# Optimization experiments

Measured on AMD Instinct MI355X. Metric: run time of the kernel, lower is better.

## Reference

```python
import jax, jax.numpy as jnp
import numpy as np
import math

D_MODEL, D_INNER, D_STATE, D_CONV, DT_RANK = 768, 1536, 16, 4, 48
BATCH, SEQLEN = 2, 1024
DT_MIN, DT_MAX = 1e-4, 1.0


def setup_inputs() -> dict:
    key = jax.random.key(0)
    ks = jax.random.split(key, 10)
    D, N, R, K = D_INNER, D_STATE, DT_RANK, D_CONV
    total_out = 2 * D + R + 2 * D * N

    def xavier(k, shape):
        fan_in, fan_out = shape[1], shape[0]
        a = math.sqrt(6.0 / (fan_in + fan_out))
        return jax.random.uniform(k, shape, jnp.float32, -a, a)

    x = jax.random.normal(ks[0], (BATCH, SEQLEN, D_MODEL), jnp.float32)
    W_in = xavier(ks[1], (total_out, D_MODEL))
    W_dt = xavier(ks[2], (D, R))
    W_out = xavier(ks[3], (D_MODEL, D))
    W_res = xavier(ks[4], (D, D_MODEL))
    conv_w = jax.random.normal(ks[5], (D, K), jnp.float32) * (1.0 / math.sqrt(K))
    conv_b = jnp.zeros((D,), jnp.float32)
    # A_log init: log(1..N) per inner channel
    A_log = jnp.broadcast_to(jnp.log(jnp.arange(1, N + 1, dtype=jnp.float32)), (D, N))
    Dskip = jnp.ones((D,), jnp.float32)
    # dt_bias = inverse_softplus(exp(uniform in [log dt_min, log dt_max]))
    dt = jnp.exp(jax.random.uniform(ks[6], (D,), jnp.float32) * (math.log(DT_MAX) - math.log(DT_MIN)) + math.log(DT_MIN))
    dt_bias = dt + jnp.log(-jnp.expm1(-dt))
    norm_w = jnp.ones((D,), jnp.float32)
    ln_w = jnp.ones((D_MODEL,), jnp.float32)
    ln_b = jnp.zeros((D_MODEL,), jnp.float32)
    return {
        "x": x, "ln_w": ln_w, "ln_b": ln_b, "W_in": W_in, "W_dt": W_dt,
        "conv_w": conv_w, "conv_b": conv_b, "A_log": A_log, "Dskip": Dskip,
        "dt_bias": dt_bias, "norm_w": norm_w, "W_res": W_res, "W_out": W_out,
    }


def _forward(x, ln_w, ln_b, W_in, W_dt, conv_w, conv_b, A_log, Dskip, dt_bias, norm_w, W_res, W_out):
    B, L, _ = x.shape
    D, N = A_log.shape
    K = conv_w.shape[1]
    R = W_dt.shape[1]
    # pre LayerNorm
    mu = x.mean(-1, keepdims=True)
    var = ((x - mu) ** 2).mean(-1, keepdims=True)
    xn = (x - mu) * jax.lax.rsqrt(var + 1e-5) * ln_w + ln_b
    # fused input projection, then split
    p = jnp.einsum('bld,od->blo', xn, W_in)  # (B,L,2D+R+2DN)
    z = p[..., :D]
    u = p[..., D:2 * D]
    dth = p[..., 2 * D:2 * D + R]
    Bpar = p[..., 2 * D + R:2 * D + R + D * N].reshape(B, L, D, N)
    Cpar = p[..., 2 * D + R + D * N:].reshape(B, L, D, N)
    # causal depthwise conv over time on u
    uc = jax.lax.conv_general_dilated(
        u.transpose(0, 2, 1), conv_w[:, None, :], (1,), [(K - 1, 0)],
        feature_group_count=D, dimension_numbers=('NCH', 'OIH', 'NCH'))
    u = (uc + conv_b[None, :, None]).transpose(0, 2, 1)  # (B,L,D)
    # dt: low-rank proj + bias -> softplus -> clamp
    dt = jnp.clip(jax.nn.softplus(jnp.einsum('blr,dr->bld', dth, W_dt) + dt_bias), DT_MIN, DT_MAX)
    A = -jnp.exp(A_log)  # (D,N), negative
    dA = jnp.exp(dt[..., None] * A)          # (B,L,D,N)
    dBu = (dt * u)[..., None] * Bpar         # (B,L,D,N)

    def step(h, inp):
        dA_t, dBu_t, C_t = inp               # each (B,D,N)
        h = dA_t * h + dBu_t
        return h, (C_t * h).sum(-1)          # y_t: (B,D)

    h0 = jnp.zeros((B, D, N), x.dtype)
    _, ys = jax.lax.scan(step, h0, (dA.transpose(1, 0, 2, 3),
                                    dBu.transpose(1, 0, 2, 3),
                                    Cpar.transpose(1, 0, 2, 3)))
    y = ys.transpose(1, 0, 2) + u * Dskip    # (B,L,D)
    # fused gated RMSNorm + inner residual
    res = jnp.einsum('blm,dm->bld', x, W_res)
    g = y * jax.nn.silu(z)
    g = g * jax.lax.rsqrt((g * g).mean(-1, keepdims=True) + 1e-6) * norm_w + res
    return jnp.einsum('bld,md->blm', g, W_out)


def reference(x, ln_w, ln_b, W_in, W_dt, conv_w, conv_b, A_log, Dskip, dt_bias, norm_w, W_res, W_out):
    return _forward(x, ln_w, ln_b, W_in, W_dt, conv_w, conv_b, A_log, Dskip, dt_bias, norm_w, W_res, W_out)
```

## Files before the change

### kernel.cpp

```cpp
#include <hip/hip_runtime.h>


typedef unsigned short u16;
typedef __bf16 bf16x8 __attribute__((ext_vector_type(8)));
typedef float f32x4 __attribute__((ext_vector_type(4)));

#define OPAD 52480
#define OTOT 52272
#define DI   1536
#define DM   768
#define Z0   0
#define U0   1536
#define DTH0 3072
#define B0   3120
#define C0   27696

#define SCAN_P 64
#define SCAN_T 16
#define SPF    4

__device__ static inline u16 f2bf(float f) {
    unsigned u = __float_as_uint(f);
    u += 0x7fffu + ((u >> 16) & 1u);
    return (u16)(u >> 16);
}
__device__ static inline float bf2f(u16 s) {
    return __uint_as_float(((unsigned)s) << 16);
}

__device__ static inline void gload16(const void* g, void* l) {
    __builtin_amdgcn_global_load_lds(
        (const __attribute__((address_space(1))) unsigned int*)g,
        (__attribute__((address_space(3))) unsigned int*)l, 16, 0, 0);
}

__device__ static inline void unpack8(uint4 v, float* f) {
    unsigned w0 = v.x, w1 = v.y, w2 = v.z, w3 = v.w;
    f[0] = __uint_as_float(w0 << 16); f[1] = __uint_as_float(w0 & 0xffff0000u);
    f[2] = __uint_as_float(w1 << 16); f[3] = __uint_as_float(w1 & 0xffff0000u);
    f[4] = __uint_as_float(w2 << 16); f[5] = __uint_as_float(w2 & 0xffff0000u);
    f[6] = __uint_as_float(w3 << 16); f[7] = __uint_as_float(w3 & 0xffff0000u);
}

__global__ void cvt_kernel(const float* __restrict__ src, u16* __restrict__ dst,
                           long n_src, long n_tot) {
    long i4 = ((long)blockIdx.x * 256 + threadIdx.x) * 4;
    if (i4 >= n_tot) return;
    ushort4 o;
    if (i4 < n_src) {
        float4 v = *(const float4*)(src + i4);
        o.x = f2bf(v.x); o.y = f2bf(v.y); o.z = f2bf(v.z); o.w = f2bf(v.w);
    } else {
        o.x = o.y = o.z = o.w = 0;
    }
    *(ushort4*)(dst + i4) = o;
}

__device__ static inline void block_reduce2(float& a, float& b) {
    #pragma unroll
    for (int o = 32; o > 0; o >>= 1) {
        a += __shfl_down(a, o);
        b += __shfl_down(b, o);
    }
    __shared__ float sa[4], sb[4];
    int lane = threadIdx.x & 63, w = threadIdx.x >> 6;
    if (lane == 0) { sa[w] = a; sb[w] = b; }
    __syncthreads();
    a = sa[0] + sa[1] + sa[2] + sa[3];
    b = sb[0] + sb[1] + sb[2] + sb[3];
}

__global__ void __launch_bounds__(256) ln_kernel(const float* __restrict__ x,
        const float* __restrict__ w, const float* __restrict__ b,
        u16* __restrict__ xnbf, u16* __restrict__ xbf) {
    int m = blockIdx.x, tid = threadIdx.x;
    const float* xr = x + (size_t)m * DM;
    float v[3];
    v[0] = xr[tid]; v[1] = xr[tid + 256]; v[2] = xr[tid + 512];
    float s = v[0] + v[1] + v[2];
    float ss = v[0]*v[0] + v[1]*v[1] + v[2]*v[2];
    block_reduce2(s, ss);
    float mu = s * (1.f / DM);
    float var = ss * (1.f / DM) - mu * mu;
    float inv = rsqrtf(var + 1e-5f);
    #pragma unroll
    for (int i = 0; i < 3; ++i) {
        int d = tid + i * 256;
        float xn = (v[i] - mu) * inv * w[d] + b[d];
        xnbf[(size_t)m * DM + d] = f2bf(xn);
        xbf[(size_t)m * DM + d] = f2bf(v[i]);
    }
}

template <int OUT_BF16>
__global__ void __launch_bounds__(256) gemm_bt(const u16* __restrict__ A,
        const u16* __restrict__ B, void* __restrict__ C, int K, int ldc) {
    __shared__ u16 smem[2 * 128 * 64];
    u16* As = smem;
    u16* Bs = smem + 128 * 64;
    int tid = threadIdx.x;
    int m0 = blockIdx.x * 128, n0 = blockIdx.y * 128;
    int lane = tid & 63, wave = tid >> 6;
    int wm = wave >> 1, wn = wave & 1;
    int l15 = lane & 15, l4 = lane >> 4;
    f32x4 acc[4][4] = {};
    const u16* Ag = A + (size_t)m0 * K;
    const u16* Bg = B + (size_t)n0 * K;
    int crow = tid >> 3;
    int ccol = ((tid & 7) ^ ((tid >> 3) & 7)) * 8;
    int ldsoff = (tid & 192) * 16;
    int xr = l15 & 7;

    for (int k0 = 0; k0 < K; k0 += 64) {
        __syncthreads();
        #pragma unroll
        for (int it = 0; it < 4; ++it) {
            gload16(Ag + (size_t)(it * 32 + crow) * K + k0 + ccol,
                    (char*)As + it * 4096 + ldsoff);
            gload16(Bg + (size_t)(it * 32 + crow) * K + k0 + ccol,
                    (char*)Bs + it * 4096 + ldsoff);
        }
        __syncthreads();
        const u16* Arow = As + (wm * 64 + l15) * 64;
        const u16* Brow = Bs + (wn * 64 + l15) * 64;
        #pragma unroll
        for (int kk8 = 0; kk8 < 8; kk8 += 4) {
            int sw = ((l4 + kk8) ^ xr) * 8;
            bf16x8 af[4], bfr[4];
            #pragma unroll
            for (int i = 0; i < 4; ++i) af[i] = *(const bf16x8*)(Arow + i * 16 * 64 + sw);
            #pragma unroll
            for (int j = 0; j < 4; ++j) bfr[j] = *(const bf16x8*)(Brow + j * 16 * 64 + sw);
            #pragma unroll
            for (int i = 0; i < 4; ++i)
                #pragma unroll
                for (int j = 0; j < 4; ++j)
                    acc[i][j] = __builtin_amdgcn_mfma_f32_16x16x32_bf16(
                        af[i], bfr[j], acc[i][j], 0, 0, 0);
        }
    }
    #pragma unroll
    for (int i = 0; i < 4; ++i) {
        int row = m0 + wm * 64 + i * 16 + l4 * 4;
        #pragma unroll
        for (int j = 0; j < 4; ++j) {
            int col = n0 + wn * 64 + j * 16 + l15;
            #pragma unroll
            for (int r = 0; r < 4; ++r) {
                size_t off = (size_t)(row + r) * ldc + col;
                if (OUT_BF16) ((u16*)C)[off] = f2bf(acc[i][j][r]);
                else          ((float*)C)[off] = acc[i][j][r];
            }
        }
    }
}

#define G2_BUF  65536
#define G2_HALF 16384
#define G2_BOFF 32768

__global__ void __launch_bounds__(512, 2) gemm256_bt(const u16* __restrict__ A,
        const u16* __restrict__ B, u16* __restrict__ C, int K, int ldc) {
    __shared__ u16 smem[65536];
    char* smemc = (char*)smem;
    const int tid = threadIdx.x;
    const int l = tid & 63, w = tid >> 6;
    const int wm = w >> 2, wn = w & 3;
    const int l15 = l & 15, l4 = l >> 4;
    const int flat = blockIdx.y * 8 + blockIdx.x;
    const int wg = (flat & 7) * 205 + (flat >> 3);
    const int m0 = (wg & 7) * 256, n0 = (wg >> 3) * 256;
    const int NT = K >> 6;

    const int rA = l15 >> 1;
    const int rdoff = rA * 128 + ((((l4 << 1) + (l15 & 1)) ^ ((rA & 3) << 1)) << 4);
    const int wpr = (l & 7) ^ (((l >> 3) & 3) << 1);
    const int srow = w * 32 + ((l >> 3) << 1) + (wpr & 1);
    const u16* Ast = A + (size_t)(m0 + srow) * K + (wpr >> 1) * 8;
    const u16* Bst = B + (size_t)(n0 + srow) * K + (wpr >> 1) * 8;
    const int sdst = w * 2048;

    f32x4 acc[8][4] = {};
    bf16x8 bvK[4];

#define G2_STAGE(MATP, MOFF, nxt, sh, tk)                                      \
    gload16(MATP + (size_t)(tk) * 64 + (sh) * 32,                              \
            smemc + (nxt) * G2_BUF + (MOFF) + (sh) * G2_HALF + sdst);          \
    gload16(MATP + (size_t)16 * K + (size_t)(tk) * 64 + (sh) * 32,             \
            smemc + (nxt) * G2_BUF + (MOFF) + (sh) * G2_HALF + sdst + 1024);

#define G2_PHASE(cur, nxt, rh, h, READB, SMAT, SMOFF, sh, tk, DO_VM)           \
    {                                                                          \
        G2_STAGE(SMAT, SMOFF, nxt, sh, tk);                                    \
        const char* Ab = smemc + (cur) * G2_BUF + (h) * G2_HALF                \
                         + (wm * 128 + (rh) * 64) * 64 + rdoff;                \
        bf16x8 af[4];                                                          \
        if (READB) {                                                           \
            const char* Bb = smemc + (cur) * G2_BUF + G2_BOFF + (h) * G2_HALF  \
                             + (wn * 64) * 64 + rdoff;                         \
            _Pragma("unroll")                                                  \
            for (int j = 0; j < 4; ++j)                                        \
                bvK[j] = *(const bf16x8*)(Bb + j * 1024);                      \
        }                                                                      \
        _Pragma("unroll")                                                      \
        for (int i = 0; i < 4; ++i) af[i] = *(const bf16x8*)(Ab + i * 1024);   \
        __builtin_amdgcn_s_barrier();                                          \
        __builtin_amdgcn_s_setprio(1);                                         \
        _Pragma("unroll")                                                      \
        for (int i = 0; i < 4; ++i)                                            \
            _Pragma("unroll")                                                  \
            for (int j = 0; j < 4; ++j)                                        \
                acc[(rh) * 4 + i][j] = __builtin_amdgcn_mfma_f32_16x16x32_bf16(\
                    af[i], bvK[j], acc[(rh) * 4 + i][j], 0, 0, 0);             \
        __builtin_amdgcn_s_setprio(0);                                         \
        if (DO_VM) asm volatile("s_waitcnt vmcnt(4)" ::: "memory");            \
        __builtin_amdgcn_s_barrier();                                          \
    }

#define G2_TILE(cur, nxt, tk)                                                  \
    G2_PHASE(cur, nxt, 0, 0, 1, Ast, 0,       0, tk, 0)                        \
    G2_PHASE(cur, nxt, 1, 0, 0, Bst, G2_BOFF, 0, tk, 1)                        \
    G2_PHASE(cur, nxt, 0, 1, 1, Ast, 0,       1, tk, 0)                        \
    G2_PHASE(cur, nxt, 1, 1, 0, Bst, G2_BOFF, 1, tk, 1)

    G2_STAGE(Ast, 0,       0, 0, 0);
    G2_STAGE(Bst, G2_BOFF, 0, 0, 0);
    G2_STAGE(Ast, 0,       0, 1, 0);
    G2_STAGE(Bst, G2_BOFF, 0, 1, 0);
    asm volatile("s_waitcnt vmcnt(4)" ::: "memory");
    __builtin_amdgcn_s_barrier();

    for (int t = 0; t < NT; t += 2) {
        int tk1 = t + 1;
        int tk2 = (t + 2 < NT) ? t + 2 : NT - 1;
        G2_TILE(0, 1, tk1)
        G2_TILE(1, 0, tk2)
    }

    #pragma unroll
    for (int ai = 0; ai < 8; ++ai) {
        int row = m0 + wm * 128 + ai * 16 + l4 * 4;
        #pragma unroll
        for (int j = 0; j < 4; ++j) {
            int col = n0 + wn * 64 + j * 16 + l15;
            #pragma unroll
            for (int r = 0; r < 4; ++r)
                C[(size_t)(row + r) * ldc + col] = f2bf(acc[ai][j][r]);
        }
    }
#undef G2_STAGE
#undef G2_PHASE
#undef G2_TILE
}

__global__ void __launch_bounds__(256) dt_kernel(const u16* __restrict__ p,
        const float* __restrict__ Wdt, const float* __restrict__ dt_bias,
        float* __restrict__ dt) {
    int m0 = blockIdx.x * 16, tid = threadIdx.x;
    __shared__ float dth_s[16 * 48];
    for (int i = tid; i < 16 * 48; i += 256)
        dth_s[i] = bf2f(p[(size_t)(m0 + i / 48) * OPAD + DTH0 + (i % 48)]);
    __syncthreads();
    #pragma unroll
    for (int ii = 0; ii < 6; ++ii) {
        int d = ii * 256 + tid;
        float base = dt_bias[d];
        float acc[16];
        #pragma unroll
        for (int mm = 0; mm < 16; ++mm) acc[mm] = base;
        for (int r = 0; r < 48; ++r) {
            float wv = Wdt[d * 48 + r];
            #pragma unroll
            for (int mm = 0; mm < 16; ++mm)
                acc[mm] = fmaf(wv, dth_s[mm * 48 + r], acc[mm]);
        }
        #pragma unroll
        for (int mm = 0; mm < 16; ++mm) {
            float xv = acc[mm];
            float sp = xv > 20.f ? xv : log1pf(__expf(xv));
            sp = fminf(fmaxf(sp, 1e-4f), 1.0f);
            dt[(size_t)(m0 + mm) * DI + d] = sp;
        }
    }
}

__global__ void __launch_bounds__(256, 2) scan1_kernel(const u16* __restrict__ p,
        const float* __restrict__ dt, const float* __restrict__ A_log,
        const float* __restrict__ cw, const float* __restrict__ cb,
        float* __restrict__ chkA, float* __restrict__ chkB) {
    int d = blockIdx.x * 256 + threadIdx.x;
    int b = blockIdx.y, c = blockIdx.z;
    int t0base = c * SCAN_T;
    float a[16];
    #pragma unroll
    for (int n = 0; n < 16; ++n) a[n] = -__expf(A_log[d * 16 + n]);
    float cw0 = cw[d*4], cw1 = cw[d*4+1], cw2 = cw[d*4+2], cw3 = cw[d*4+3];
    float cbv = cb[d];
    const u16* pB = p + (size_t)(b * 1024 + t0base) * OPAD + B0 + d * 16;
    const u16* pU = p + (size_t)(b * 1024 + t0base) * OPAD + U0 + d;
    const float* dtp = dt + (size_t)(b * 1024 + t0base) * DI + d;
    float x1, x2, x3;
    if (c == 0) { x1 = x2 = x3 = 0.f; }
    else {
        x1 = bf2f(*(pU - (long)OPAD));
        x2 = bf2f(*(pU - 2L * OPAD));
        x3 = bf2f(*(pU - 3L * OPAD));
    }
    uint4 Br[SPF][2]; float dtr[SPF], xur[SPF];
    #pragma unroll
    for (int i = 0; i < SPF; ++i) {
        Br[i][0] = *(const uint4*)(pB + (size_t)i * OPAD);
        Br[i][1] = *(const uint4*)(pB + (size_t)i * OPAD + 8);
        dtr[i] = dtp[(size_t)i * DI];
        xur[i] = bf2f(pU[(size_t)i * OPAD]);
    }
    float h[16], Av[16];
    #pragma unroll
    for (int n = 0; n < 16; ++n) { h[n] = 0.f; Av[n] = 1.f; }
    for (int t0 = 0; t0 < SCAN_T; t0 += SPF) {
        #pragma unroll
        for (int s = 0; s < SPF; ++s) {
            int t = t0 + s;
            uint4 b0 = Br[s][0], b1 = Br[s][1];
            float dtv = dtr[s], xt = xur[s];
            int tl = t + SPF < SCAN_T ? t + SPF : SCAN_T - 1;
            Br[s][0] = *(const uint4*)(pB + (size_t)tl * OPAD);
            Br[s][1] = *(const uint4*)(pB + (size_t)tl * OPAD + 8);
            dtr[s] = dtp[(size_t)tl * DI];
            xur[s] = bf2f(pU[(size_t)tl * OPAD]);
            float uv = cbv;
            uv = fmaf(cw0, x3, uv);
            uv = fmaf(cw1, x2, uv);
            uv = fmaf(cw2, x1, uv);
            uv = fmaf(cw3, xt, uv);
            x3 = x2; x2 = x1; x1 = xt;
            float Bf[16];
            unpack8(b0, Bf); unpack8(b1, Bf + 8);
            float dtu = dtv * uv;
            #pragma unroll
            for (int n = 0; n < 16; ++n) {
                float dA = __expf(dtv * a[n]);
                h[n] = fmaf(dA, h[n], dtu * Bf[n]);
                Av[n] *= dA;
            }
        }
    }
    size_t o = (((size_t)c * 2 + b) * 1536 + d) * 16;
    #pragma unroll
    for (int k = 0; k < 4; ++k) {
        *(float4*)(chkA + o + k * 4) = make_float4(Av[4*k], Av[4*k+1], Av[4*k+2], Av[4*k+3]);
        *(float4*)(chkB + o + k * 4) = make_float4(h[4*k], h[4*k+1], h[4*k+2], h[4*k+3]);
    }
}

__global__ void __launch_bounds__(256) scan_comb_kernel(const float* __restrict__ chkA,
        const float* __restrict__ chkB, float* __restrict__ hstart) {
    int idx = blockIdx.x * 256 + threadIdx.x;
    float hs = 0.f;
    for (int c = 0; c < SCAN_P; ++c) {
        size_t o = (size_t)c * 49152 + idx;
        hstart[o] = hs;
        hs = fmaf(chkA[o], hs, chkB[o]);
    }
}

__global__ void __launch_bounds__(256, 2) scan2_kernel(const u16* __restrict__ p,
        const float* __restrict__ dt, const float* __restrict__ A_log,
        const float* __restrict__ cw, const float* __restrict__ cb,
        const float* __restrict__ Dskip,
        const float* __restrict__ hstart, float* __restrict__ y) {
    int d = blockIdx.x * 256 + threadIdx.x;
    int b = blockIdx.y, c = blockIdx.z;
    int t0base = c * SCAN_T;
    float a[16];
    #pragma unroll
    for (int n = 0; n < 16; ++n) a[n] = -__expf(A_log[d * 16 + n]);
    float Dsk = Dskip[d];
    float cw0 = cw[d*4], cw1 = cw[d*4+1], cw2 = cw[d*4+2], cw3 = cw[d*4+3];
    float cbv = cb[d];
    const u16* pB = p + (size_t)(b * 1024 + t0base) * OPAD + B0 + d * 16;
    const u16* pC = p + (size_t)(b * 1024 + t0base) * OPAD + C0 + d * 16;
    const u16* pU = p + (size_t)(b * 1024 + t0base) * OPAD + U0 + d;
    const float* dtp = dt + (size_t)(b * 1024 + t0base) * DI + d;
    float* yp        = y  + (size_t)(b * 1024 + t0base) * DI + d;
    float x1, x2, x3;
    if (c == 0) { x1 = x2 = x3 = 0.f; }
    else {
        x1 = bf2f(*(pU - (long)OPAD));
        x2 = bf2f(*(pU - 2L * OPAD));
        x3 = bf2f(*(pU - 3L * OPAD));
    }
    uint4 Br[SPF][2], Cr[SPF][2]; float dtr[SPF], xur[SPF];
    #pragma unroll
    for (int i = 0; i < SPF; ++i) {
        Br[i][0] = *(const uint4*)(pB + (size_t)i * OPAD);
        Br[i][1] = *(const uint4*)(pB + (size_t)i * OPAD + 8);
        Cr[i][0] = *(const uint4*)(pC + (size_t)i * OPAD);
        Cr[i][1] = *(const uint4*)(pC + (size_t)i * OPAD + 8);
        dtr[i] = dtp[(size_t)i * DI];
        xur[i] = bf2f(pU[(size_t)i * OPAD]);
    }
    float h[16];
    {
        size_t o = ((size_t)c * 3072 + (size_t)b * 1536 + d) * 16;
        #pragma unroll
        for (int k = 0; k < 4; ++k) {
            float4 hv = *(const float4*)(hstart + o + k * 4);
            h[4*k] = hv.x; h[4*k+1] = hv.y; h[4*k+2] = hv.z; h[4*k+3] = hv.w;
        }
    }
    for (int t0 = 0; t0 < SCAN_T; t0 += SPF) {
        #pragma unroll
        for (int s = 0; s < SPF; ++s) {
            int t = t0 + s;
            uint4 b0 = Br[s][0], b1 = Br[s][1], c0 = Cr[s][0], c1 = Cr[s][1];
            float dtv = dtr[s], xt = xur[s];
            int tl = t + SPF < SCAN_T ? t + SPF : SCAN_T - 1;
            Br[s][0] = *(const uint4*)(pB + (size_t)tl * OPAD);
            Br[s][1] = *(const uint4*)(pB + (size_t)tl * OPAD + 8);
            Cr[s][0] = *(const uint4*)(pC + (size_t)tl * OPAD);
            Cr[s][1] = *(const uint4*)(pC + (size_t)tl * OPAD + 8);
            dtr[s] = dtp[(size_t)tl * DI];
            xur[s] = bf2f(pU[(size_t)tl * OPAD]);
            float uv = cbv;
            uv = fmaf(cw0, x3, uv);
            uv = fmaf(cw1, x2, uv);
            uv = fmaf(cw2, x1, uv);
            uv = fmaf(cw3, xt, uv);
            x3 = x2; x2 = x1; x1 = xt;
            float Bf[16], Cf[16];
            unpack8(b0, Bf); unpack8(b1, Bf + 8);
            unpack8(c0, Cf); unpack8(c1, Cf + 8);
            float dtu = dtv * uv;
            #pragma unroll
            for (int n = 0; n < 16; ++n) {
                float dA = __expf(dtv * a[n]);
                h[n] = fmaf(dA, h[n], dtu * Bf[n]);
            }
            float a0 = fmaf(Cf[0], h[0], uv * Dsk), a1 = Cf[1] * h[1];
            float a2 = Cf[2] * h[2], a3 = Cf[3] * h[3];
            #pragma unroll
            for (int n = 4; n < 16; n += 4) {
                a0 = fmaf(Cf[n],   h[n],   a0);
                a1 = fmaf(Cf[n+1], h[n+1], a1);
                a2 = fmaf(Cf[n+2], h[n+2], a2);
                a3 = fmaf(Cf[n+3], h[n+3], a3);
            }
            yp[(size_t)t * DI] = (a0 + a1) + (a2 + a3);
        }
    }
}

__global__ void __launch_bounds__(256) gate_kernel(const u16* __restrict__ p,
        const float* __restrict__ y, const float* __restrict__ res,
        const float* __restrict__ norm_w, u16* __restrict__ g) {
    int m = blockIdx.x, tid = threadIdx.x;
    const u16* pz = p + (size_t)m * OPAD + Z0;
    const float* yr = y + (size_t)m * DI;
    float gp[6];
    float ss = 0.f, dummy = 0.f;
    #pragma unroll
    for (int i = 0; i < 6; ++i) {
        int d = i * 256 + tid;
        float z = bf2f(pz[d]);
        float gv = yr[d] * z / (1.f + __expf(-z));
        gp[i] = gv;
        ss += gv * gv;
    }
    block_reduce2(ss, dummy);
    float scale = rsqrtf(ss * (1.f / DI) + 1e-6f);
    #pragma unroll
    for (int i = 0; i < 6; ++i) {
        int d = i * 256 + tid;
        float val = gp[i] * scale * norm_w[d] + res[(size_t)m * DI + d];
        g[(size_t)m * DI + d] = f2bf(val);
    }
}

extern "C" void kernel_launch(void* const* d_in, const int* in_sizes, int n_in,
                              void* d_out, int out_size, void* d_ws, size_t ws_size,
                              hipStream_t stream) {
    const float* x       = (const float*)d_in[0];
    const float* ln_w    = (const float*)d_in[1];
    const float* ln_b    = (const float*)d_in[2];
    const float* W_in    = (const float*)d_in[3];
    const float* W_dt    = (const float*)d_in[4];
    const float* conv_w  = (const float*)d_in[5];
    const float* conv_b  = (const float*)d_in[6];
    const float* A_log   = (const float*)d_in[7];
    const float* Dskip   = (const float*)d_in[8];
    const float* dt_bias = (const float*)d_in[9];
    const float* norm_w  = (const float*)d_in[10];
    const float* W_res   = (const float*)d_in[11];
    const float* W_out   = (const float*)d_in[12];
    float* out = (float*)d_out;

    char* wsb = (char*)d_ws;
    u16* Wbf     = (u16*)(wsb + 0);
    u16* Wresbf  = (u16*)(wsb + 80609280);
    u16* Woutbf  = (u16*)(wsb + 82968576);
    u16* xnbf    = (u16*)(wsb + 85327872);
    u16* xbf     = (u16*)(wsb + 88473600);
    u16* pbuf    = (u16*)(wsb + 91619328);
    float* dtv   = (float*)(wsb + 319160320);
    float* ybuf  = (float*)(wsb + 331743232);
    float* resb  = (float*)(wsb + 344326144);
    u16* gbuf    = (u16*)(wsb + 356909056);
    float* chkA  = (float*)(wsb + 0);
    float* chkB  = (float*)(wsb + 12582912);
    float* hst   = (float*)(wsb + 25165824);

    cvt_kernel<<<39360, 256, 0, stream>>>(W_in, Wbf, (long)OTOT * DM, (long)OPAD * DM);
    cvt_kernel<<<1152, 256, 0, stream>>>(W_res, Wresbf, (long)DI * DM, (long)DI * DM);
    cvt_kernel<<<1152, 256, 0, stream>>>(W_out, Woutbf, (long)DM * DI, (long)DM * DI);
    ln_kernel<<<2048, 256, 0, stream>>>(x, ln_w, ln_b, xnbf, xbf);
    gemm256_bt<<<dim3(8, 205), 512, 0, stream>>>(xnbf, Wbf, pbuf, DM, OPAD);
    gemm_bt<0><<<dim3(16, 12), 256, 0, stream>>>(xbf, Wresbf, resb, DM, DI);
    dt_kernel<<<128, 256, 0, stream>>>(pbuf, W_dt, dt_bias, dtv);
    scan1_kernel<<<dim3(6, 2, SCAN_P), 256, 0, stream>>>(pbuf, dtv, A_log, conv_w, conv_b, chkA, chkB);
    scan_comb_kernel<<<192, 256, 0, stream>>>(chkA, chkB, hst);
    scan2_kernel<<<dim3(6, 2, SCAN_P), 256, 0, stream>>>(pbuf, dtv, A_log, conv_w, conv_b, Dskip, hst, ybuf);
    gate_kernel<<<2048, 256, 0, stream>>>(pbuf, ybuf, resb, norm_w, gbuf);
    gemm_bt<0><<<dim3(16, 6), 256, 0, stream>>>(gbuf, Woutbf, out, DI, DM);
}
```

Measured before the change: 691.4 us.

## Merge GEMM phases into two per tile and spread dt kernel over more blocks

The main 256x256 GEMM now runs two phases per K-tile instead of four. Each phase stages both the A and B halves and loads both A row-halves plus B from shared memory, then issues 32 MFMAs between barriers. This halves the barriers and the vmcnt waits per tile, at the cost of more live fragment registers and a deeper load burst. Separately, dt_kernel handles 4 rows per block instead of 16 and launches 512 blocks rather than 128, which raises parallelism but re-reads W_dt more often.

```diff
diff --git a/kernel.cpp b/kernel.cpp
--- a/kernel.cpp
+++ b/kernel.cpp
@@ -181,7 +181,6 @@
     const int sdst = w * 2048;
 
     f32x4 acc[8][4] = {};
-    bf16x8 bvK[4];
 
 #define G2_STAGE(MATP, MOFF, nxt, sh, tk)                                      \
     gload16(MATP + (size_t)(tk) * 64 + (sh) * 32,                              \
@@ -189,39 +188,44 @@
     gload16(MATP + (size_t)16 * K + (size_t)(tk) * 64 + (sh) * 32,             \
             smemc + (nxt) * G2_BUF + (MOFF) + (sh) * G2_HALF + sdst + 1024);
 
-#define G2_PHASE(cur, nxt, rh, h, READB, SMAT, SMOFF, sh, tk, DO_VM)           \
+#define G2_PHASE(cur, nxt, h, tk)                                              \
     {                                                                          \
-        G2_STAGE(SMAT, SMOFF, nxt, sh, tk);                                    \
+        G2_STAGE(Ast, 0,       nxt, h, tk);                                    \
+        G2_STAGE(Bst, G2_BOFF, nxt, h, tk);                                    \
         const char* Ab = smemc + (cur) * G2_BUF + (h) * G2_HALF                \
-                         + (wm * 128 + (rh) * 64) * 64 + rdoff;                \
-        bf16x8 af[4];                                                          \
-        if (READB) {                                                           \
-            const char* Bb = smemc + (cur) * G2_BUF + G2_BOFF + (h) * G2_HALF  \
-                             + (wn * 64) * 64 + rdoff;                         \
-            _Pragma("unroll")                                                  \
-            for (int j = 0; j < 4; ++j)                                        \
-                bvK[j] = *(const bf16x8*)(Bb + j * 1024);                      \
+                         + (wm * 128) * 64 + rdoff;                            \
+        const char* Bb = smemc + (cur) * G2_BUF + G2_BOFF + (h) * G2_HALF      \
+                         + (wn * 64) * 64 + rdoff;                             \
+        bf16x8 af0[4], af1[4], bv[4];                                          \
+        _Pragma("unroll")                                                      \
+        for (int j = 0; j < 4; ++j) bv[j] = *(const bf16x8*)(Bb + j * 1024);   \
+        _Pragma("unroll")                                                      \
+        for (int i = 0; i < 4; ++i) {                                          \
+            af0[i] = *(const bf16x8*)(Ab + i * 1024);                          \
+            af1[i] = *(const bf16x8*)(Ab + 4096 + i * 1024);                   \
         }                                                                      \
-        _Pragma("unroll")                                                      \
-        for (int i = 0; i < 4; ++i) af[i] = *(const bf16x8*)(Ab + i * 1024);   \
         __builtin_amdgcn_s_barrier();                                          \
         __builtin_amdgcn_s_setprio(1);                                         \
         _Pragma("unroll")                                                      \
         for (int i = 0; i < 4; ++i)                                            \
             _Pragma("unroll")                                                  \
             for (int j = 0; j < 4; ++j)                                        \
-                acc[(rh) * 4 + i][j] = __builtin_amdgcn_mfma_f32_16x16x32_bf16(\
-                    af[i], bvK[j], acc[(rh) * 4 + i][j], 0, 0, 0);             \
+                acc[i][j] = __builtin_amdgcn_mfma_f32_16x16x32_bf16(           \
+                    af0[i], bv[j], acc[i][j], 0, 0, 0);                        \
+        _Pragma("unroll")                                                      \
+        for (int i = 0; i < 4; ++i)                                            \
+            _Pragma("unroll")                                                  \
+            for (int j = 0; j < 4; ++j)                                        \
+                acc[4 + i][j] = __builtin_amdgcn_mfma_f32_16x16x32_bf16(       \
+                    af1[i], bv[j], acc[4 + i][j], 0, 0, 0);                    \
         __builtin_amdgcn_s_setprio(0);                                         \
-        if (DO_VM) asm volatile("s_waitcnt vmcnt(4)" ::: "memory");            \
+        asm volatile("s_waitcnt vmcnt(4)" ::: "memory");                       \
         __builtin_amdgcn_s_barrier();                                          \
     }
 
 #define G2_TILE(cur, nxt, tk)                                                  \
-    G2_PHASE(cur, nxt, 0, 0, 1, Ast, 0,       0, tk, 0)                        \
-    G2_PHASE(cur, nxt, 1, 0, 0, Bst, G2_BOFF, 0, tk, 1)                        \
-    G2_PHASE(cur, nxt, 0, 1, 1, Ast, 0,       1, tk, 0)                        \
-    G2_PHASE(cur, nxt, 1, 1, 0, Bst, G2_BOFF, 1, tk, 1)
+    G2_PHASE(cur, nxt, 0, tk)                                                  \
+    G2_PHASE(cur, nxt, 1, tk)
 
     G2_STAGE(Ast, 0,       0, 0, 0);
     G2_STAGE(Bst, G2_BOFF, 0, 0, 0);
@@ -256,26 +260,26 @@
 __global__ void __launch_bounds__(256) dt_kernel(const u16* __restrict__ p,
         const float* __restrict__ Wdt, const float* __restrict__ dt_bias,
         float* __restrict__ dt) {
-    int m0 = blockIdx.x * 16, tid = threadIdx.x;
-    __shared__ float dth_s[16 * 48];
-    for (int i = tid; i < 16 * 48; i += 256)
+    int m0 = blockIdx.x * 4, tid = threadIdx.x;
+    __shared__ float dth_s[4 * 48];
+    for (int i = tid; i < 4 * 48; i += 256)
         dth_s[i] = bf2f(p[(size_t)(m0 + i / 48) * OPAD + DTH0 + (i % 48)]);
     __syncthreads();
     #pragma unroll
     for (int ii = 0; ii < 6; ++ii) {
         int d = ii * 256 + tid;
         float base = dt_bias[d];
-        float acc[16];
-        #pragma unroll
-        for (int mm = 0; mm < 16; ++mm) acc[mm] = base;
+        float acc[4];
+        #pragma unroll
+        for (int mm = 0; mm < 4; ++mm) acc[mm] = base;
         for (int r = 0; r < 48; ++r) {
             float wv = Wdt[d * 48 + r];
             #pragma unroll
-            for (int mm = 0; mm < 16; ++mm)
+            for (int mm = 0; mm < 4; ++mm)
                 acc[mm] = fmaf(wv, dth_s[mm * 48 + r], acc[mm]);
         }
         #pragma unroll
-        for (int mm = 0; mm < 16; ++mm) {
+        for (int mm = 0; mm < 4; ++mm) {
             float xv = acc[mm];
             float sp = xv > 20.f ? xv : log1pf(__expf(xv));
             sp = fminf(fmaxf(sp, 1e-4f), 1.0f);
@@ -516,7 +520,7 @@
     ln_kernel<<<2048, 256, 0, stream>>>(x, ln_w, ln_b, xnbf, xbf);
     gemm256_bt<<<dim3(8, 205), 512, 0, stream>>>(xnbf, Wbf, pbuf, DM, OPAD);
     gemm_bt<0><<<dim3(16, 12), 256, 0, stream>>>(xbf, Wresbf, resb, DM, DI);
-    dt_kernel<<<128, 256, 0, stream>>>(pbuf, W_dt, dt_bias, dtv);
+    dt_kernel<<<512, 256, 0, stream>>>(pbuf, W_dt, dt_bias, dtv);
     scan1_kernel<<<dim3(6, 2, SCAN_P), 256, 0, stream>>>(pbuf, dtv, A_log, conv_w, conv_b, chkA, chkB);
     scan_comb_kernel<<<192, 256, 0, stream>>>(chkA, chkB, hst);
     scan2_kernel<<<dim3(6, 2, SCAN_P), 256, 0, stream>>>(pbuf, dtv, A_log, conv_w, conv_b, Dskip, hst, ybuf);
```

Measured after the change: 664.9 us. -3.8%, faster.
